# Performance work log

Hardware: AMD Instinct MI355X
Metric: run time of the kernel (lower is better)

The kernel has to match this reference:

```python
import jax, jax.numpy as jnp
import numpy as np

WINDOW_SIZE = 11
SIGMA = 1.5
C1 = 0.01 ** 2
C2 = 0.03 ** 2


def _gaussian_window(channels):
    coords = jnp.arange(WINDOW_SIZE, dtype=jnp.float32) - WINDOW_SIZE // 2
    g = jnp.exp(-coords ** 2 / (2.0 * SIGMA ** 2))
    g = g / g.sum()
    w2d = g[:, None] * g[None, :]                      # [K, K]
    # depthwise kernel: [out_ch=C, in_ch/groups=1, K, K]
    return jnp.broadcast_to(w2d[None, None], (channels, 1, WINDOW_SIZE, WINDOW_SIZE))


def _depthwise_conv(x, window):
    # x: [B, C, H, W]; grouped conv with feature_group_count = C, SAME padding
    C = x.shape[1]
    pad = WINDOW_SIZE // 2
    return jax.lax.conv_general_dilated(
        x, window,
        window_strides=(1, 1),
        padding=((pad, pad), (pad, pad)),
        dimension_numbers=("NCHW", "OIHW", "NCHW"),
        feature_group_count=C,
    )


def setup_inputs() -> dict:
    key = jax.random.key(0)
    k1, k2 = jax.random.split(key)
    shape = (16, 3, 512, 512)
    pred = jax.random.uniform(k1, shape, dtype=jnp.float32)
    target = jax.random.uniform(k2, shape, dtype=jnp.float32)
    return {"pred": pred, "target": target}


def reference(pred, target):
    C = pred.shape[1]
    window = _gaussian_window(C)
    mu_p = _depthwise_conv(pred, window)
    mu_t = _depthwise_conv(target, window)
    mu_p_sq = mu_p ** 2
    mu_t_sq = mu_t ** 2
    mu_cross = mu_p * mu_t
    sigma_p_sq = _depthwise_conv(pred ** 2, window) - mu_p_sq
    sigma_t_sq = _depthwise_conv(target ** 2, window) - mu_t_sq
    sigma_cross = _depthwise_conv(pred * target, window) - mu_cross
    ssim_map = ((2.0 * mu_cross + C1) * (2.0 * sigma_cross + C2)) / (
        (mu_p_sq + mu_t_sq + C1) * (sigma_p_sq + sigma_t_sq + C2)
    )
    return 1.0 - ssim_map.mean()
```

## Files before the change

### kernel.cpp

```cpp
#include <hip/hip_runtime.h>

#define HH 512
#define WW 512
#define NPLANE 48
#define BY 128
#define CHK 16
#define NCH (BY / CHK)
#define RING 32
#define PSTR 40
#define KS 11

typedef __attribute__((ext_vector_type(8))) short short8;
typedef __attribute__((ext_vector_type(4))) float floatx4;
typedef __attribute__((ext_vector_type(2))) float float2v;
typedef __attribute__((ext_vector_type(2))) __bf16 bf16x2v;

__device__ inline unsigned pk2bf_rne(float a, float b) {
    union { float f; unsigned u; } ua, ub;
    ua.f = a; ub.f = b;
    unsigned lo = (ua.u + 0x7FFFu + ((ua.u >> 16) & 1u)) >> 16;
    unsigned hi = (ub.u + 0x7FFFu + ((ub.u >> 16) & 1u)) >> 16;
    return lo | (hi << 16);
}

__device__ inline unsigned pkbf2(float2v f) {
    bf16x2v v = __builtin_convertvector(f, bf16x2v);
    return __builtin_bit_cast(unsigned, v);
}

struct Raw { float4 p0, p1, t0, t1; };

__global__ __launch_bounds__(256, 4) void ssim_kernel(
    const float* __restrict__ pred, const float* __restrict__ target,
    float* __restrict__ ws_sum)
{
    __shared__ __align__(16) short ring[4][4][16][PSTR];

    const int tid = threadIdx.x;
    const int wv = tid >> 6;
    const int lane = tid & 63;
    const int m = lane & 15;
    const int quad = lane >> 4;

    float wsum = 0.f;
#pragma unroll
    for (int k = 0; k < KS; ++k) {
        float d = (float)(k - 5);
        wsum += __expf(-d * d * (1.0f / 4.5f));
    }
    const float invs = 1.0f / wsum;

    short8 Wf;
    {
        union { short8 v; unsigned u[4]; } W;
#pragma unroll
        for (int jj = 0; jj < 4; ++jj) {
            float v0, v1;
            {
                int idx = quad * 8 + 2 * jj - m - 3;
                float d = (float)(idx - 5);
                v0 = (idx >= 0 && idx < KS) ? __expf(-d * d * (1.0f / 4.5f)) * invs : 0.f;
            }
            {
                int idx = quad * 8 + 2 * jj + 1 - m - 3;
                float d = (float)(idx - 5);
                v1 = (idx >= 0 && idx < KS) ? __expf(-d * d * (1.0f / 4.5f)) * invs : 0.f;
            }
            W.u[jj] = pk2bf_rne(v0, v1);
        }
        Wf = W.v;
    }

    const size_t poff = (size_t)blockIdx.z * HH * WW;
    const int X0 = blockIdx.x * 64 + wv * 16;
    const int rawX = X0 - 8;
    const int Y0 = blockIdx.y * BY;

    const int c0 = rawX + quad * 8;
    const bool okc0 = (unsigned)c0 < (unsigned)WW;
    const bool okc1 = (unsigned)(c0 + 4) < (unsigned)WW;
    const float* __restrict__ pc = pred + poff + c0;
    const float* __restrict__ tc = target + poff + c0;

    const float2v C1v = {1.0e-4f, 1.0e-4f};
    const float2v C2v = {9.0e-4f, 9.0e-4f};
    float lsum = 0.f;
    const floatx4 z = {0.f, 0.f, 0.f, 0.f};

    auto load_raw = [&](int k) -> Raw {
        Raw r;
        r.p0 = make_float4(0, 0, 0, 0); r.p1 = make_float4(0, 0, 0, 0);
        r.t0 = make_float4(0, 0, 0, 0); r.t1 = make_float4(0, 0, 0, 0);
        const int row = Y0 + CHK * k - 8 + m;
        if ((unsigned)row < (unsigned)HH) {
            const float* pr = pc + (size_t)row * WW;
            const float* tr = tc + (size_t)row * WW;
            if (okc0) { r.p0 = *(const float4*)pr;      r.t0 = *(const float4*)tr; }
            if (okc1) { r.p1 = *(const float4*)(pr + 4); r.t1 = *(const float4*)(tr + 4); }
        }
        return r;
    };

    auto h_step = [&](const Raw& r, int sb) {
        const float2v pa[4] = {{r.p0.x, r.p0.y}, {r.p0.z, r.p0.w},
                               {r.p1.x, r.p1.y}, {r.p1.z, r.p1.w}};
        const float2v tb[4] = {{r.t0.x, r.t0.y}, {r.t0.z, r.t0.w},
                               {r.t1.x, r.t1.y}, {r.t1.z, r.t1.w}};
        union { short8 v; unsigned u[4]; } Fp, Ft, Fq, Fpt;
#pragma unroll
        for (int jj = 0; jj < 4; ++jj) {
            Fp.u[jj]  = pkbf2(pa[jj]);
            Ft.u[jj]  = pkbf2(tb[jj]);
            Fq.u[jj]  = pkbf2(pa[jj] * pa[jj] + tb[jj] * tb[jj]);
            Fpt.u[jj] = pkbf2(pa[jj] * tb[jj]);
        }
        floatx4 Dp  = __builtin_amdgcn_mfma_f32_16x16x32_bf16(Fp.v,  Wf, z, 0, 0, 0);
        floatx4 Dt  = __builtin_amdgcn_mfma_f32_16x16x32_bf16(Ft.v,  Wf, z, 0, 0, 0);
        floatx4 Dq  = __builtin_amdgcn_mfma_f32_16x16x32_bf16(Fq.v,  Wf, z, 0, 0, 0);
        floatx4 Dpt = __builtin_amdgcn_mfma_f32_16x16x32_bf16(Fpt.v, Wf, z, 0, 0, 0);
        const int slot = (sb + quad * 4) & (RING - 1);
        uint2 v;
        v.x = pkbf2(float2v{Dp[0],  Dp[1]});  v.y = pkbf2(float2v{Dp[2],  Dp[3]});
        *(uint2*)&ring[wv][0][m][slot] = v;
        v.x = pkbf2(float2v{Dt[0],  Dt[1]});  v.y = pkbf2(float2v{Dt[2],  Dt[3]});
        *(uint2*)&ring[wv][1][m][slot] = v;
        v.x = pkbf2(float2v{Dq[0],  Dq[1]});  v.y = pkbf2(float2v{Dq[2],  Dq[3]});
        *(uint2*)&ring[wv][2][m][slot] = v;
        v.x = pkbf2(float2v{Dpt[0], Dpt[1]}); v.y = pkbf2(float2v{Dpt[2], Dpt[3]});
        *(uint2*)&ring[wv][3][m][slot] = v;
    };

    short8 Bp, Bt, Bq, Bpt;
    auto vread = [&](int base) {
        const int sq = (base + quad * 8) & (RING - 1);
        Bp  = *(const short8*)&ring[wv][0][m][sq];
        Bt  = *(const short8*)&ring[wv][1][m][sq];
        Bq  = *(const short8*)&ring[wv][2][m][sq];
        Bpt = *(const short8*)&ring[wv][3][m][sq];
    };

    auto vfin = [&]() {
        floatx4 Mp  = __builtin_amdgcn_mfma_f32_16x16x32_bf16(Wf, Bp,  z, 0, 0, 0);
        floatx4 Mt  = __builtin_amdgcn_mfma_f32_16x16x32_bf16(Wf, Bt,  z, 0, 0, 0);
        floatx4 Mq  = __builtin_amdgcn_mfma_f32_16x16x32_bf16(Wf, Bq,  z, 0, 0, 0);
        floatx4 Mpt = __builtin_amdgcn_mfma_f32_16x16x32_bf16(Wf, Bpt, z, 0, 0, 0);
#pragma unroll
        for (int h = 0; h < 2; ++h) {
            const float2v mup = {Mp[2*h],  Mp[2*h+1]};
            const float2v mut = {Mt[2*h],  Mt[2*h+1]};
            const float2v mq  = {Mq[2*h],  Mq[2*h+1]};
            const float2v mpt = {Mpt[2*h], Mpt[2*h+1]};
            const float2v mupsq = mup * mup, mutsq = mut * mut, mucr = mup * mut;
            const float2v scr = mpt - mucr;
            const float2v n1 = mucr + mucr + C1v;
            const float2v n2 = scr + scr + C2v;
            const float2v d1 = mupsq + mutsq + C1v;
            const float2v d2 = (mq - mupsq - mutsq) + C2v;
            const float2v num = n1 * n2, den = d1 * d2;
            lsum += __fdividef(num[0], den[0]) + __fdividef(num[1], den[1]);
        }
    };

    {
        Raw A = load_raw(0);
        Raw B = load_raw(1);
        h_step(A, 24);
        h_step(B, 8);
    }
    Raw C = load_raw(2);
    Raw D = load_raw(3);

#pragma unroll 1
    for (int ii = 0; ii < 4; ii += 2) {
        vread(24);
        h_step(C, 24);
        C = load_raw(ii + 4);
        vfin();

        vread(8);
        h_step(D, 8);
        D = load_raw(ii + 5);
        vfin();
    }
    vread(24);
    h_step(C, 24);
    C = load_raw(8);
    vfin();
    vread(8);
    h_step(D, 8);
    vfin();
    vread(24);
    h_step(C, 24);
    vfin();
    vread(8);
    vfin();

#pragma unroll
    for (int off = 32; off > 0; off >>= 1) lsum += __shfl_down(lsum, off, 64);
    if (lane == 0) *(float*)&ring[wv][0][0][0] = lsum;
    __syncthreads();
    if (tid == 0) {
        atomicAdd(ws_sum, *(const float*)&ring[0][0][0][0]
                        + *(const float*)&ring[1][0][0][0]
                        + *(const float*)&ring[2][0][0][0]
                        + *(const float*)&ring[3][0][0][0]);
    }
}

__global__ void finalize_kernel(const float* __restrict__ ws_sum,
                                float* __restrict__ out) {
    out[0] = 1.0f - ws_sum[0] * (1.0f / 12582912.0f);
}

extern "C" void kernel_launch(void* const* d_in, const int* in_sizes, int n_in,
                              void* d_out, int out_size, void* d_ws, size_t ws_size,
                              hipStream_t stream) {
    const float* pred = (const float*)d_in[0];
    const float* target = (const float*)d_in[1];
    float* out = (float*)d_out;
    float* ws = (float*)d_ws;

    hipMemsetAsync(ws, 0, sizeof(float), stream);
    dim3 grid(WW / 64, HH / BY, NPLANE);
    ssim_kernel<<<grid, 256, 0, stream>>>(pred, target, ws);
    finalize_kernel<<<1, 1, 0, stream>>>(ws, out);
}
```

Before: 143.0 us.

## Process two column strips per wave with interleaved independent pipelines

Each wave now handles two 16-column strips (block width 128 instead of 64), running two independent horizontal/vertical MFMA pipelines with separate LDS rings, interleaved in the same loop. This adds instruction-level parallelism to hide MFMA and load latency, halves the grid size and amortizes the per-block Gaussian weight setup. In exchange it raises register and LDS use per block, which may lower occupancy, and leaves fewer blocks to spread across CUs.

```diff
diff --git a/kernel.cpp b/kernel.cpp
--- a/kernel.cpp
+++ b/kernel.cpp
@@ -4,8 +4,8 @@
 #define WW 512
 #define NPLANE 48
 #define BY 128
+#define BX 128
 #define CHK 16
-#define NCH (BY / CHK)
 #define RING 32
 #define PSTR 40
 #define KS 11
@@ -28,13 +28,15 @@
     return __builtin_bit_cast(unsigned, v);
 }
 
-struct Raw { float4 p0, p1, t0, t1; };
+struct Raw   { float4 p0, p1, t0, t1; };
+struct Frags { short8 p, t, q, pt; };
 
 __global__ __launch_bounds__(256, 4) void ssim_kernel(
     const float* __restrict__ pred, const float* __restrict__ target,
     float* __restrict__ ws_sum)
 {
-    __shared__ __align__(16) short ring[4][4][16][PSTR];
+    __shared__ __align__(16) short ring[4][2][4][16][PSTR];
+    __shared__ float red[4];
 
     const int tid = threadIdx.x;
     const int wv = tid >> 6;
@@ -72,22 +74,27 @@
     }
 
     const size_t poff = (size_t)blockIdx.z * HH * WW;
-    const int X0 = blockIdx.x * 64 + wv * 16;
-    const int rawX = X0 - 8;
     const int Y0 = blockIdx.y * BY;
 
-    const int c0 = rawX + quad * 8;
-    const bool okc0 = (unsigned)c0 < (unsigned)WW;
-    const bool okc1 = (unsigned)(c0 + 4) < (unsigned)WW;
-    const float* __restrict__ pc = pred + poff + c0;
-    const float* __restrict__ tc = target + poff + c0;
+    const int XA = blockIdx.x * BX + wv * 16;
+    const int cA = XA - 8 + quad * 8;
+    const int cB = cA + 64;
+    const bool okA0 = (unsigned)cA < (unsigned)WW;
+    const bool okA1 = (unsigned)(cA + 4) < (unsigned)WW;
+    const bool okB0 = (unsigned)cB < (unsigned)WW;
+    const bool okB1 = (unsigned)(cB + 4) < (unsigned)WW;
+    const float* __restrict__ pcA = pred + poff + cA;
+    const float* __restrict__ tcA = target + poff + cA;
+    const float* __restrict__ pcB = pred + poff + cB;
+    const float* __restrict__ tcB = target + poff + cB;
 
     const float2v C1v = {1.0e-4f, 1.0e-4f};
     const float2v C2v = {9.0e-4f, 9.0e-4f};
     float lsum = 0.f;
     const floatx4 z = {0.f, 0.f, 0.f, 0.f};
 
-    auto load_raw = [&](int k) -> Raw {
+    auto load_raw = [&](const float* __restrict__ pc, const float* __restrict__ tc,
+                        bool ok0, bool ok1, int k) -> Raw {
         Raw r;
         r.p0 = make_float4(0, 0, 0, 0); r.p1 = make_float4(0, 0, 0, 0);
         r.t0 = make_float4(0, 0, 0, 0); r.t1 = make_float4(0, 0, 0, 0);
@@ -95,13 +102,13 @@
         if ((unsigned)row < (unsigned)HH) {
             const float* pr = pc + (size_t)row * WW;
             const float* tr = tc + (size_t)row * WW;
-            if (okc0) { r.p0 = *(const float4*)pr;      r.t0 = *(const float4*)tr; }
-            if (okc1) { r.p1 = *(const float4*)(pr + 4); r.t1 = *(const float4*)(tr + 4); }
+            if (ok0) { r.p0 = *(const float4*)pr;       r.t0 = *(const float4*)tr; }
+            if (ok1) { r.p1 = *(const float4*)(pr + 4); r.t1 = *(const float4*)(tr + 4); }
         }
         return r;
     };
 
-    auto h_step = [&](const Raw& r, int sb) {
+    auto h_step = [&](int pipe, const Raw& r, int sb) {
         const float2v pa[4] = {{r.p0.x, r.p0.y}, {r.p0.z, r.p0.w},
                                {r.p1.x, r.p1.y}, {r.p1.z, r.p1.w}};
         const float2v tb[4] = {{r.t0.x, r.t0.y}, {r.t0.z, r.t0.w},
@@ -121,29 +128,30 @@
         const int slot = (sb + quad * 4) & (RING - 1);
         uint2 v;
         v.x = pkbf2(float2v{Dp[0],  Dp[1]});  v.y = pkbf2(float2v{Dp[2],  Dp[3]});
-        *(uint2*)&ring[wv][0][m][slot] = v;
+        *(uint2*)&ring[wv][pipe][0][m][slot] = v;
         v.x = pkbf2(float2v{Dt[0],  Dt[1]});  v.y = pkbf2(float2v{Dt[2],  Dt[3]});
-        *(uint2*)&ring[wv][1][m][slot] = v;
+        *(uint2*)&ring[wv][pipe][1][m][slot] = v;
         v.x = pkbf2(float2v{Dq[0],  Dq[1]});  v.y = pkbf2(float2v{Dq[2],  Dq[3]});
-        *(uint2*)&ring[wv][2][m][slot] = v;
+        *(uint2*)&ring[wv][pipe][2][m][slot] = v;
         v.x = pkbf2(float2v{Dpt[0], Dpt[1]}); v.y = pkbf2(float2v{Dpt[2], Dpt[3]});
-        *(uint2*)&ring[wv][3][m][slot] = v;
-    };
-
-    short8 Bp, Bt, Bq, Bpt;
-    auto vread = [&](int base) {
+        *(uint2*)&ring[wv][pipe][3][m][slot] = v;
+    };
+
+    auto vread = [&](int pipe, int base) -> Frags {
         const int sq = (base + quad * 8) & (RING - 1);
-        Bp  = *(const short8*)&ring[wv][0][m][sq];
-        Bt  = *(const short8*)&ring[wv][1][m][sq];
-        Bq  = *(const short8*)&ring[wv][2][m][sq];
-        Bpt = *(const short8*)&ring[wv][3][m][sq];
-    };
-
-    auto vfin = [&]() {
-        floatx4 Mp  = __builtin_amdgcn_mfma_f32_16x16x32_bf16(Wf, Bp,  z, 0, 0, 0);
-        floatx4 Mt  = __builtin_amdgcn_mfma_f32_16x16x32_bf16(Wf, Bt,  z, 0, 0, 0);
-        floatx4 Mq  = __builtin_amdgcn_mfma_f32_16x16x32_bf16(Wf, Bq,  z, 0, 0, 0);
-        floatx4 Mpt = __builtin_amdgcn_mfma_f32_16x16x32_bf16(Wf, Bpt, z, 0, 0, 0);
+        Frags f;
+        f.p  = *(const short8*)&ring[wv][pipe][0][m][sq];
+        f.t  = *(const short8*)&ring[wv][pipe][1][m][sq];
+        f.q  = *(const short8*)&ring[wv][pipe][2][m][sq];
+        f.pt = *(const short8*)&ring[wv][pipe][3][m][sq];
+        return f;
+    };
+
+    auto vfin = [&](const Frags& f) {
+        floatx4 Mp  = __builtin_amdgcn_mfma_f32_16x16x32_bf16(Wf, f.p,  z, 0, 0, 0);
+        floatx4 Mt  = __builtin_amdgcn_mfma_f32_16x16x32_bf16(Wf, f.t,  z, 0, 0, 0);
+        floatx4 Mq  = __builtin_amdgcn_mfma_f32_16x16x32_bf16(Wf, f.q,  z, 0, 0, 0);
+        floatx4 Mpt = __builtin_amdgcn_mfma_f32_16x16x32_bf16(Wf, f.pt, z, 0, 0, 0);
 #pragma unroll
         for (int h = 0; h < 2; ++h) {
             const float2v mup = {Mp[2*h],  Mp[2*h+1]};
@@ -161,49 +169,52 @@
         }
     };
 
+    Raw CA, CB;
+    CA = load_raw(pcA, tcA, okA0, okA1, 0);
+    CB = load_raw(pcB, tcB, okB0, okB1, 0);
+    h_step(0, CA, 24); h_step(1, CB, 24);
+    CA = load_raw(pcA, tcA, okA0, okA1, 1);
+    CB = load_raw(pcB, tcB, okB0, okB1, 1);
+    h_step(0, CA, 8);  h_step(1, CB, 8);
+    CA = load_raw(pcA, tcA, okA0, okA1, 2);
+    CB = load_raw(pcB, tcB, okB0, okB1, 2);
+
+#pragma unroll 1
+    for (int ii = 0; ii < 6; ii += 2) {
+        {
+            Frags FA = vread(0, 24), FB = vread(1, 24);
+            h_step(0, CA, 24);
+            h_step(1, CB, 24);
+            CA = load_raw(pcA, tcA, okA0, okA1, ii + 3);
+            CB = load_raw(pcB, tcB, okB0, okB1, ii + 3);
+            vfin(FA); vfin(FB);
+        }
+        {
+            Frags FA = vread(0, 8), FB = vread(1, 8);
+            h_step(0, CA, 8);
+            h_step(1, CB, 8);
+            CA = load_raw(pcA, tcA, okA0, okA1, ii + 4);
+            CB = load_raw(pcB, tcB, okB0, okB1, ii + 4);
+            vfin(FA); vfin(FB);
+        }
+    }
     {
-        Raw A = load_raw(0);
-        Raw B = load_raw(1);
-        h_step(A, 24);
-        h_step(B, 8);
-    }
-    Raw C = load_raw(2);
-    Raw D = load_raw(3);
-
-#pragma unroll 1
-    for (int ii = 0; ii < 4; ii += 2) {
-        vread(24);
-        h_step(C, 24);
-        C = load_raw(ii + 4);
-        vfin();
-
-        vread(8);
-        h_step(D, 8);
-        D = load_raw(ii + 5);
-        vfin();
-    }
-    vread(24);
-    h_step(C, 24);
-    C = load_raw(8);
-    vfin();
-    vread(8);
-    h_step(D, 8);
-    vfin();
-    vread(24);
-    h_step(C, 24);
-    vfin();
-    vread(8);
-    vfin();
+        Frags FA = vread(0, 24), FB = vread(1, 24);
+        h_step(0, CA, 24);
+        h_step(1, CB, 24);
+        vfin(FA); vfin(FB);
+    }
+    {
+        Frags FA = vread(0, 8), FB = vread(1, 8);
+        vfin(FA); vfin(FB);
+    }
 
 #pragma unroll
     for (int off = 32; off > 0; off >>= 1) lsum += __shfl_down(lsum, off, 64);
-    if (lane == 0) *(float*)&ring[wv][0][0][0] = lsum;
+    if (lane == 0) red[wv] = lsum;
     __syncthreads();
     if (tid == 0) {
-        atomicAdd(ws_sum, *(const float*)&ring[0][0][0][0]
-                        + *(const float*)&ring[1][0][0][0]
-                        + *(const float*)&ring[2][0][0][0]
-                        + *(const float*)&ring[3][0][0][0]);
+        atomicAdd(ws_sum, red[0] + red[1] + red[2] + red[3]);
     }
 }
 
@@ -221,7 +232,7 @@
     float* ws = (float*)d_ws;
 
     hipMemsetAsync(ws, 0, sizeof(float), stream);
-    dim3 grid(WW / 64, HH / BY, NPLANE);
+    dim3 grid(WW / BX, HH / BY, NPLANE);
     ssim_kernel<<<grid, 256, 0, stream>>>(pred, target, ws);
     finalize_kernel<<<1, 1, 0, stream>>>(ws, out);
 }
```

Measured after the change: 144.6 us. Within noise of the previous version (+1.1%).
